# Optimization experiments

Hardware: AMD Instinct MI355X
Metric: run time of the kernel (lower is better)

## Reference

```python
import jax, jax.numpy as jnp
import numpy as np

B, S, D, H, EXP = 4, 2048, 768, 8, 4
HD = D // H  # head dim = 96
EPS = 1e-5


def layer_norm(x, g, b):
    mu = jnp.mean(x, axis=-1, keepdims=True)
    var = jnp.mean(jnp.square(x - mu), axis=-1, keepdims=True)
    return (x - mu) * jax.lax.rsqrt(var + EPS) * g + b


def setup_inputs() -> dict:
    key = jax.random.key(0)
    ks = jax.random.split(key, 16)
    s = 0.02
    f32 = jnp.float32
    x = jax.random.normal(ks[0], (B, S, D), f32)
    Wq = jax.random.normal(ks[1], (D, D), f32) * s
    bq = jnp.zeros((D,), f32)
    Wk = jax.random.normal(ks[2], (D, D), f32) * s
    bk = jnp.zeros((D,), f32)
    Wv = jax.random.normal(ks[3], (D, D), f32) * s
    bv = jnp.zeros((D,), f32)
    Wo = jax.random.normal(ks[4], (D, D), f32) * s
    bo = jnp.zeros((D,), f32)
    g1 = jnp.ones((D,), f32)
    be1 = jnp.zeros((D,), f32)
    W1 = jax.random.normal(ks[5], (D, D * EXP), f32) * s
    bf1 = jnp.zeros((D * EXP,), f32)
    W2 = jax.random.normal(ks[6], (D * EXP, D), f32) * s
    bf2 = jnp.zeros((D,), f32)
    g2 = jnp.ones((D,), f32)
    be2 = jnp.zeros((D,), f32)
    return dict(x=x, Wq=Wq, bq=bq, Wk=Wk, bk=bk, Wv=Wv, bv=bv, Wo=Wo, bo=bo,
                g1=g1, be1=be1, W1=W1, bf1=bf1, W2=W2, bf2=bf2, g2=g2, be2=be2)


def reference(x, Wq, bq, Wk, bk, Wv, bv, Wo, bo, g1, be1, W1, bf1, W2, bf2, g2, be2):
    scale = HD ** (-0.5)
    # multi-head attention (manual QK^T softmax V)
    q = (x @ Wq + bq).reshape(B, S, H, HD).transpose(0, 2, 1, 3)  # b H s c
    k = (x @ Wk + bk).reshape(B, S, H, HD).transpose(0, 2, 1, 3)
    v = (x @ Wv + bv).reshape(B, S, H, HD).transpose(0, 2, 1, 3)
    scores = jnp.einsum('bhqc,bhkc->bhqk', q, k) * scale
    attn = jax.nn.softmax(scores, axis=-1)
    o = jnp.einsum('bhqk,bhkc->bhqc', attn, v)
    o = o.transpose(0, 2, 1, 3).reshape(B, S, D)
    attn_out = o @ Wo + bo
    # residual + LN
    x1 = layer_norm(attn_out + x, g1, be1)
    # feed-forward with GELU
    h = jax.nn.gelu(x1 @ W1 + bf1)
    ffn_out = h @ W2 + bf2
    # residual + LN
    return layer_norm(ffn_out + x1, g2, be2)
```

## Files before the change

kernel.cpp:

```cpp
#include <hip/hip_runtime.h>
#include <hip/hip_bf16.h>
#include <math.h>
#include <stdint.h>

#define B_    4
#define S_    2048
#define D_    768
#define H_    8
#define HD_   96
#define EXPD_ 3072
#define MSZ   8192

#define QSCALE 0.14724439f
#define M0_    12.0f

typedef __bf16 bf16;
typedef __bf16 bf16x4 __attribute__((ext_vector_type(4)));
typedef __bf16 bf16x8 __attribute__((ext_vector_type(8)));
typedef float  f32x4  __attribute__((ext_vector_type(4)));
typedef float  f32x16 __attribute__((ext_vector_type(16)));

typedef __attribute__((address_space(1))) const uint32_t gu32;
typedef __attribute__((address_space(3))) uint32_t lu32;

__device__ __forceinline__ void async_copy16(const void* g, void* l) {
    __builtin_amdgcn_global_load_lds((gu32*)g, (lu32*)l, 16, 0, 0);
}

__device__ __forceinline__ float gelu_f(float x) {
    float x3 = x * x * x;
    return 0.5f * x * (1.0f + tanhf(0.7978845608028654f * (x + 0.044715f * x3)));
}

__device__ __forceinline__ bool sniff_f32(const void* p) {
    const bf16* pb = (const bf16*)p;
    float v = (float)pb[2 * (threadIdx.x & 63)];
    bool big = !(fabsf(v) < 1000.0f);
    return __any(big) != 0;
}

__device__ __forceinline__ float dynld(const void* p, size_t i, bool f32in) {
    return f32in ? ((const float*)p)[i] : (float)((const bf16*)p)[i];
}

__global__ __launch_bounds__(256) void cast_kernel(
    const void* __restrict__ src, bf16* __restrict__ dst)
{
    const bool f32in = sniff_f32(src);
    size_t i = ((size_t)blockIdx.x * 256 + threadIdx.x) * 8;
    if (f32in) {
        f32x4 a = *(const f32x4*)((const float*)src + i);
        f32x4 b = *(const f32x4*)((const float*)src + i + 4);
        bf16x8 r;
#pragma unroll
        for (int e = 0; e < 4; ++e) { r[e] = (bf16)a[e]; r[e + 4] = (bf16)b[e]; }
        *(bf16x8*)(dst + i) = r;
    } else {
        *(bf16x8*)(dst + i) = *(const bf16x8*)((const bf16*)src + i);
    }
}

#define MODE_QKV  0
#define MODE_RES  1
#define MODE_GELU 2

template<int MODE, bool ADYN, bool RESDYN, int BN>
__global__ __launch_bounds__(256) void gemm2_kernel(
    const void* __restrict__ A, const bf16* __restrict__ Bt,
    const void* __restrict__ b0, const void* __restrict__ b1, const void* __restrict__ b2,
    const void* __restrict__ res, bf16* __restrict__ out,
    int M, int N, int K, int lda, int ldb, int boff, int mstripe,
    const void* __restrict__ sniffp)
{
    constexpr int WN   = BN / 2;
    constexpr int NJ32 = WN / 32;
    constexpr int BSZ  = BN * 32;
    __shared__ __align__(16) bf16 Sh[8192 + 2 * BSZ];
    bf16* Asp[2] = { Sh, Sh + 4096 };
    bf16* Bsp[2] = { Sh + 8192, Sh + 8192 + BSZ };

    const bool f32in = sniff_f32(sniffp);
    const int tid  = threadIdx.x;
    const int w    = tid >> 6;
    const int lane = tid & 63;
    const int l32  = lane & 31;
    const int kh   = lane >> 5;
    const int wr   = w >> 1, wc = w & 1;

    const int lin  = blockIdx.x;
    const int xcd  = lin & 7;
    const int q    = lin >> 3;
    const int nb   = q / mstripe;
    const int mbin = q - nb * mstripe;
    const int m0   = (xcd * mstripe + mbin) * 128;
    const int n0   = nb * BN;

    const int rsub = lane >> 2;
    const int cb8  = (lane & 3) * 8;

    f32x16 acc[2][NJ32];
#pragma unroll
    for (int i = 0; i < 2; ++i)
#pragma unroll
        for (int j = 0; j < NJ32; ++j)
#pragma unroll
            for (int e = 0; e < 16; ++e) acc[i][j][e] = 0.f;

    const bf16*  Abf = (const bf16*)A;
    const float* Af  = (const float*)A;

    for (int k0 = 0; k0 < K; k0 += 64) {
        __syncthreads();
#pragma unroll
        for (int half = 0; half < 2; ++half) {
            if (ADYN && f32in) {
#pragma unroll
                for (int a = 0; a < 2; ++a) {
                    int row = w * 32 + a * 16 + rsub;
                    const float* sp = Af + (size_t)(m0 + row) * lda + k0 + half * 32 + cb8;
                    f32x4 u0 = *(const f32x4*)sp;
                    f32x4 u1 = *(const f32x4*)(sp + 4);
                    bf16x8 v;
#pragma unroll
                    for (int e = 0; e < 4; ++e) { v[e] = (bf16)u0[e]; v[e + 4] = (bf16)u1[e]; }
                    *(bf16x8*)(&Asp[half][(size_t)(w * 32 + a * 16) * 32 + lane * 8]) = v;
                }
            } else {
#pragma unroll
                for (int a = 0; a < 2; ++a) {
                    int row = w * 32 + a * 16 + rsub;
                    async_copy16(Abf + (size_t)(m0 + row) * lda + k0 + half * 32 + cb8,
                                 &Asp[half][(w * 32 + a * 16) * 32]);
                }
            }
#pragma unroll
            for (int a = 0; a < BN / 64; ++a) {
                int row = w * (BN / 4) + a * 16 + rsub;
                async_copy16(Bt + (size_t)(n0 + row) * ldb + k0 + half * 32 + cb8,
                             &Bsp[half][(w * (BN / 4) + a * 16) * 32]);
            }
        }
        __syncthreads();

#pragma unroll
        for (int hs = 0; hs < 2; ++hs) {
            bf16x8 af[2][2], bfv[NJ32][2];
#pragma unroll
            for (int i = 0; i < 2; ++i)
#pragma unroll
                for (int ks = 0; ks < 2; ++ks)
                    af[i][ks] = *(const bf16x8*)(&Asp[hs][(wr * 64 + i * 32 + l32) * 32 + ks * 16 + kh * 8]);
#pragma unroll
            for (int j = 0; j < NJ32; ++j)
#pragma unroll
                for (int ks = 0; ks < 2; ++ks)
                    bfv[j][ks] = *(const bf16x8*)(&Bsp[hs][(wc * WN + j * 32 + l32) * 32 + ks * 16 + kh * 8]);
#pragma unroll
            for (int i = 0; i < 2; ++i)
#pragma unroll
                for (int j = 0; j < NJ32; ++j)
#pragma unroll
                    for (int ks = 0; ks < 2; ++ks)
                        acc[i][j] = __builtin_amdgcn_mfma_f32_32x32x16_bf16(af[i][ks], bfv[j][ks], acc[i][j], 0, 0, 0);
        }
    }

    if constexpr (MODE == MODE_QKV) {
#pragma unroll
        for (int j = 0; j < NJ32; ++j) {
            int nbase = n0 + wc * WN + j * 32;
            int which = nbase / D_;
            int n2b   = nbase - which * D_;
            int h     = n2b / HD_;
            int hd0   = n2b - h * HD_;
            const void* bp = which == 0 ? b0 : (which == 1 ? b1 : b2);
            float bval = dynld(bp, n2b + l32, f32in);
            int hd = hd0 + l32;
#pragma unroll
            for (int i = 0; i < 2; ++i) {
#pragma unroll
                for (int g = 0; g < 16; ++g) {
                    int rr = (g & 3) + 8 * (g >> 2) + 4 * kh;
                    int m  = m0 + wr * 64 + i * 32 + rr;
                    float v = acc[i][j][g] + bval;
                    int b  = m >> 11;
                    int ss = m & (S_ - 1);
                    int bh = b * H_ + h;
                    if (which == 0) v *= QSCALE;
                    size_t dst;
                    if (which < 2)
                        dst = (size_t)which * (MSZ * D_) + ((size_t)bh * S_ + ss) * HD_ + hd;
                    else
                        dst = (size_t)2 * (MSZ * D_) + ((size_t)bh * HD_ + hd) * S_ + ss;
                    out[dst] = (bf16)v;
                }
            }
        }
    } else {
        __syncthreads();
        bf16* Cw = Sh + w * 2048;
        for (int j = 0; j < NJ32; ++j) {
            int nl = n0 + wc * WN + j * 32 + l32;
            float bval = boff >= 0 ? dynld(b0, boff + nl, f32in) : 0.f;
#pragma unroll
            for (int i = 0; i < 2; ++i)
#pragma unroll
                for (int g = 0; g < 16; ++g) {
                    int rr = (g & 3) + 8 * (g >> 2) + 4 * kh;
                    float v = acc[i][j][g] + bval;
                    if constexpr (MODE == MODE_GELU) v = gelu_f(v);
                    Cw[(i * 32 + rr) * 32 + l32] = (bf16)v;
                }
#pragma unroll
            for (int pass = 0; pass < 4; ++pass) {
                int row = pass * 16 + (lane >> 2);
                int cc  = (lane & 3) * 8;
                bf16x8 cv = *(const bf16x8*)&Cw[row * 32 + cc];
                int m = m0 + wr * 64 + row;
                int n = n0 + wc * WN + j * 32 + cc;
                size_t off = (size_t)m * N + n;
                if constexpr (MODE == MODE_RES) {
                    bf16x8 o;
                    if (RESDYN && f32in) {
                        f32x4 r0 = *(const f32x4*)((const float*)res + off);
                        f32x4 r1 = *(const f32x4*)((const float*)res + off + 4);
#pragma unroll
                        for (int e = 0; e < 4; ++e) {
                            o[e]     = (bf16)((float)cv[e] + r0[e]);
                            o[e + 4] = (bf16)((float)cv[e + 4] + r1[e]);
                        }
                    } else {
                        bf16x8 rv = *(const bf16x8*)((const bf16*)res + off);
#pragma unroll
                        for (int e = 0; e < 8; ++e) o[e] = (bf16)((float)cv[e] + (float)rv[e]);
                    }
                    *(bf16x8*)&out[off] = o;
                } else {
                    *(bf16x8*)&out[off] = cv;
                }
            }
        }
    }
}

__global__ __launch_bounds__(256, 2) void flash_kernel(
    const bf16* __restrict__ Q, const bf16* __restrict__ Kk,
    const bf16* __restrict__ Vt_g, bf16* __restrict__ ctx)
{
    __shared__ __align__(16) bf16 Ks[64][104];
    __shared__ __align__(16) bf16 Vs[96][72];
    __shared__ __align__(16) bf16 Ps[4][32][72];

    const int tid  = threadIdx.x;
    const int w    = tid >> 6;
    const int lane = tid & 63;
    const int quad = lane >> 4;
    const int l16  = lane & 15;
    const int bh   = blockIdx.x;
    const size_t base = (size_t)bh * S_ * HD_;
    const int q0   = blockIdx.y * 128 + w * 32;

    bf16x8 qf[2][3];
#pragma unroll
    for (int qs = 0; qs < 2; ++qs)
#pragma unroll
        for (int ch = 0; ch < 3; ++ch)
            qf[qs][ch] = *(const bf16x8*)(Q + base + (size_t)(q0 + qs * 16 + l16) * HD_ + ch * 32 + quad * 8);

    f32x4 oacc[2][6];
#pragma unroll
    for (int qs = 0; qs < 2; ++qs)
#pragma unroll
        for (int c = 0; c < 6; ++c) oacc[qs][c] = (f32x4){0.f, 0.f, 0.f, 0.f};
    float lsum[2] = {0.f, 0.f};

    int krow[3], kc8[3], vrow[3], vc8[3];
#pragma unroll
    for (int i = 0; i < 3; ++i) {
        int id = tid + i * 256;
        krow[i] = id / 12; kc8[i] = (id - krow[i] * 12) * 8;
        vrow[i] = id >> 3; vc8[i] = (id & 7) * 8;
    }

    bf16x8 kreg[3], vreg[3];
#pragma unroll
    for (int i = 0; i < 3; ++i) {
        kreg[i] = *(const bf16x8*)(Kk + base + (size_t)krow[i] * HD_ + kc8[i]);
        vreg[i] = *(const bf16x8*)(Vt_g + base + (size_t)vrow[i] * S_ + vc8[i]);
    }
#pragma unroll
    for (int i = 0; i < 3; ++i) {
        *(bf16x8*)(&Ks[krow[i]][kc8[i]]) = kreg[i];
        *(bf16x8*)(&Vs[vrow[i]][vc8[i]]) = vreg[i];
    }
    __syncthreads();

    for (int kv0 = 0; kv0 < S_; kv0 += 64) {
        const bool more = (kv0 + 64) < S_;
        if (more) {
#pragma unroll
            for (int i = 0; i < 3; ++i) {
                kreg[i] = *(const bf16x8*)(Kk + base + (size_t)(kv0 + 64 + krow[i]) * HD_ + kc8[i]);
                vreg[i] = *(const bf16x8*)(Vt_g + base + (size_t)vrow[i] * S_ + kv0 + 64 + vc8[i]);
            }
        }

        f32x4 sacc[2][4];
#pragma unroll
        for (int qs = 0; qs < 2; ++qs)
#pragma unroll
            for (int t = 0; t < 4; ++t)
                sacc[qs][t] = (f32x4){-M0_, -M0_, -M0_, -M0_};
#pragma unroll
        for (int t = 0; t < 4; ++t)
#pragma unroll
            for (int ch = 0; ch < 3; ++ch) {
                bf16x8 kf = *(const bf16x8*)(&Ks[t * 16 + l16][ch * 32 + quad * 8]);
                sacc[0][t] = __builtin_amdgcn_mfma_f32_16x16x32_bf16(kf, qf[0][ch], sacc[0][t], 0, 0, 0);
                sacc[1][t] = __builtin_amdgcn_mfma_f32_16x16x32_bf16(kf, qf[1][ch], sacc[1][t], 0, 0, 0);
            }

#pragma unroll
        for (int qs = 0; qs < 2; ++qs) {
            bf16* prow = &Ps[w][qs * 16 + l16][quad * 4];
#pragma unroll
            for (int t = 0; t < 4; ++t) {
                float p0 = exp2f(sacc[qs][t][0]);
                float p1 = exp2f(sacc[qs][t][1]);
                float p2 = exp2f(sacc[qs][t][2]);
                float p3 = exp2f(sacc[qs][t][3]);
                lsum[qs] += (p0 + p1) + (p2 + p3);
                bf16x4 pv;
                pv[0] = (bf16)p0; pv[1] = (bf16)p1; pv[2] = (bf16)p2; pv[3] = (bf16)p3;
                *(bf16x4*)(prow + t * 16) = pv;
            }
        }

        bf16x8 pf[2][2];
#pragma unroll
        for (int qs = 0; qs < 2; ++qs) {
            pf[qs][0] = *(const bf16x8*)(&Ps[w][qs * 16 + l16][quad * 8]);
            pf[qs][1] = *(const bf16x8*)(&Ps[w][qs * 16 + l16][32 + quad * 8]);
        }
#pragma unroll
        for (int c = 0; c < 6; ++c) {
            bf16x8 vf0 = *(const bf16x8*)(&Vs[c * 16 + l16][quad * 8]);
            bf16x8 vf1 = *(const bf16x8*)(&Vs[c * 16 + l16][32 + quad * 8]);
            oacc[0][c] = __builtin_amdgcn_mfma_f32_16x16x32_bf16(pf[0][0], vf0, oacc[0][c], 0, 0, 0);
            oacc[0][c] = __builtin_amdgcn_mfma_f32_16x16x32_bf16(pf[0][1], vf1, oacc[0][c], 0, 0, 0);
            oacc[1][c] = __builtin_amdgcn_mfma_f32_16x16x32_bf16(pf[1][0], vf0, oacc[1][c], 0, 0, 0);
            oacc[1][c] = __builtin_amdgcn_mfma_f32_16x16x32_bf16(pf[1][1], vf1, oacc[1][c], 0, 0, 0);
        }

        if (more) {
            __syncthreads();
#pragma unroll
            for (int i = 0; i < 3; ++i) {
                *(bf16x8*)(&Ks[krow[i]][kc8[i]]) = kreg[i];
                *(bf16x8*)(&Vs[vrow[i]][vc8[i]]) = vreg[i];
            }
            __syncthreads();
        }
    }

#pragma unroll
    for (int qs = 0; qs < 2; ++qs) {
        lsum[qs] += __shfl_xor(lsum[qs], 16);
        lsum[qs] += __shfl_xor(lsum[qs], 32);
    }
    const int b = bh >> 3, h = bh & 7;
#pragma unroll
    for (int qs = 0; qs < 2; ++qs)
#pragma unroll
        for (int r = 0; r < 4; ++r) {
            float inv = 1.0f / __shfl(lsum[qs], quad * 4 + r);
            int srow = q0 + qs * 16 + quad * 4 + r;
            size_t rowbase = ((size_t)b * S_ + srow) * D_ + h * HD_;
#pragma unroll
            for (int c = 0; c < 6; ++c)
                ctx[rowbase + c * 16 + l16] = (bf16)(oacc[qs][c][r] * inv);
        }
}

template<bool OUTDYN>
__global__ __launch_bounds__(256) void ln_kernel(
    const bf16* __restrict__ in, const void* __restrict__ g, const void* __restrict__ be,
    void* __restrict__ out, const void* __restrict__ sniffp)
{
    const bool f32in = sniff_f32(sniffp);
    const int w = threadIdx.x >> 6, lane = threadIdx.x & 63;
    const int row = blockIdx.x * 4 + w;
    const size_t rbase = (size_t)row * D_ + lane * 12;

    float v[12];
#pragma unroll
    for (int j = 0; j < 3; ++j) {
        bf16x4 t = *(const bf16x4*)(in + rbase + j * 4);
#pragma unroll
        for (int e = 0; e < 4; ++e) v[j * 4 + e] = (float)t[e];
    }
    float sum = 0.f;
#pragma unroll
    for (int j = 0; j < 12; ++j) sum += v[j];
#pragma unroll
    for (int off = 1; off < 64; off <<= 1) sum += __shfl_xor(sum, off);
    float mu = sum * (1.0f / D_);
    float sq = 0.f;
#pragma unroll
    for (int j = 0; j < 12; ++j) { v[j] -= mu; sq += v[j] * v[j]; }
#pragma unroll
    for (int off = 1; off < 64; off <<= 1) sq += __shfl_xor(sq, off);
    float rstd = rsqrtf(sq * (1.0f / D_) + 1e-5f);

    if (OUTDYN && f32in) {
        float* op = (float*)out + rbase;
#pragma unroll
        for (int j = 0; j < 3; ++j) {
            f32x4 t;
#pragma unroll
            for (int e = 0; e < 4; ++e) {
                int c = lane * 12 + j * 4 + e;
                t[e] = v[j * 4 + e] * rstd * dynld(g, c, true) + dynld(be, c, true);
            }
            *(f32x4*)(op + j * 4) = t;
        }
    } else {
        bf16* op = (bf16*)out + rbase;
#pragma unroll
        for (int j = 0; j < 3; ++j) {
            bf16x4 t;
#pragma unroll
            for (int e = 0; e < 4; ++e) {
                int c = lane * 12 + j * 4 + e;
                t[e] = (bf16)(v[j * 4 + e] * rstd * dynld(g, c, f32in) + dynld(be, c, f32in));
            }
            *(bf16x4*)(op + j * 4) = t;
        }
    }
}

__device__ __forceinline__ void transpose_tile(
    const void* __restrict__ src, bf16* __restrict__ dst, int R, int C,
    int r0, int c0, bool f32in)
{
    __shared__ bf16 t[64][65];
    const int tx = threadIdx.x & 63, ty = threadIdx.x >> 6;
#pragma unroll
    for (int i = 0; i < 16; ++i) {
        int rr = ty + i * 4;
        t[rr][tx] = (bf16)dynld(src, (size_t)(r0 + rr) * C + c0 + tx, f32in);
    }
    __syncthreads();
#pragma unroll
    for (int i = 0; i < 16; ++i) {
        int cc = ty + i * 4;
        dst[(size_t)(c0 + cc) * R + r0 + tx] = t[tx][cc];
    }
}

__global__ __launch_bounds__(256) void transpose_qkv_kernel(
    const void* __restrict__ s0, const void* __restrict__ s1, const void* __restrict__ s2,
    bf16* __restrict__ dst)
{
    const void* src = blockIdx.z == 0 ? s0 : (blockIdx.z == 1 ? s1 : s2);
    const bool f32in = sniff_f32(src);
    transpose_tile(src, dst + (size_t)blockIdx.z * D_ * D_, D_, D_,
                   blockIdx.y * 64, blockIdx.x * 64, f32in);
}

__global__ __launch_bounds__(256) void transpose_mlp_kernel(
    const void* __restrict__ s0, const void* __restrict__ s1, const void* __restrict__ s2,
    bf16* __restrict__ dst)
{
    int id = blockIdx.x;
    const void* src;
    int R, C, r, c;
    size_t off;
    if (id < 144)      { src = s0; R = D_;    C = D_;    off = 0;
                         r = id / 12;          c = id % 12; }
    else if (id < 720) { src = s1; R = D_;    C = EXPD_; off = (size_t)D_ * D_;
                         int i = id - 144;     r = i / 48; c = i % 48; }
    else               { src = s2; R = EXPD_; C = D_;    off = (size_t)D_ * D_ + (size_t)D_ * EXPD_;
                         int i = id - 720;     r = i / 12; c = i % 12; }
    const bool f32in = sniff_f32(src);
    transpose_tile(src, dst + off, R, C, r * 64, c * 64, f32in);
}

extern "C" void kernel_launch(void* const* d_in, const int* in_sizes, int n_in,
                              void* d_out, int out_size, void* d_ws, size_t ws_size,
                              hipStream_t stream)
{
    (void)in_sizes; (void)n_in; (void)out_size;
    const void* x   = d_in[0];
    const void* Wq  = d_in[1];
    const void* bq  = d_in[2];
    const void* Wk  = d_in[3];
    const void* bk  = d_in[4];
    const void* Wv  = d_in[5];
    const void* bv  = d_in[6];
    const void* Wo  = d_in[7];
    const void* bo  = d_in[8];
    const void* g1  = d_in[9];
    const void* be1 = d_in[10];
    const void* W1  = d_in[11];
    const void* bf1 = d_in[12];
    const void* W2  = d_in[13];
    const void* bf2 = d_in[14];
    const void* g2  = d_in[15];
    const void* be2 = d_in[16];

    const size_t REG = (size_t)MSZ * D_ * 2;
    char* p = (char*)d_ws;
    bf16* R0 = (bf16*)p;
    bf16* R1 = (bf16*)(p + REG);
    bf16* R2 = (bf16*)(p + 2 * REG);
    bf16* R3 = (bf16*)(p + 3 * REG);
    bf16* R4 = (bf16*)(p + 4 * REG);

    int tier = 0;
    if      (ws_size >= 9 * REG) tier = 3;
    else if (ws_size >= 5 * REG) tier = 1;
    bf16* xb = tier == 3 ? (bf16*)(p + 8 * REG) : R4;

    bf16* qkvT = (bf16*)d_out;
    bf16* ctx  = (bf16*)d_out;
    dim3 blk(256);
    const int MB8 = MSZ / 128 / 8;

    if (tier >= 1) cast_kernel<<<dim3(MSZ * D_ / (256 * 8)), blk, 0, stream>>>(x, xb);

    transpose_qkv_kernel<<<dim3(12, 12, 3), blk, 0, stream>>>(Wq, Wk, Wv, qkvT);

    if (tier >= 1)
        gemm2_kernel<MODE_QKV, false, false, 128><<<dim3(64 * 18), blk, 0, stream>>>(
            xb, qkvT, bq, bk, bv, nullptr, R0, MSZ, 2304, D_, D_, D_, 0, MB8, Wq);
    else
        gemm2_kernel<MODE_QKV, true, false, 128><<<dim3(64 * 18), blk, 0, stream>>>(
            x, qkvT, bq, bk, bv, nullptr, R0, MSZ, 2304, D_, D_, D_, 0, MB8, Wq);

    flash_kernel<<<dim3(B_ * H_, S_ / 128), dim3(256), 0, stream>>>(R0, R1, R2, ctx);

    bf16* WoT = R1;
    bf16* W1T = WoT + (size_t)D_ * D_;
    bf16* W2T = W1T + (size_t)D_ * EXPD_;
    transpose_mlp_kernel<<<dim3(1296), blk, 0, stream>>>(Wo, W1, W2, WoT);

    if (tier >= 1)
        gemm2_kernel<MODE_RES, false, false, 64><<<dim3(64 * 12), blk, 0, stream>>>(
            ctx, WoT, bo, nullptr, nullptr, xb, R3, MSZ, D_, D_, D_, D_, 0, MB8, Wq);
    else
        gemm2_kernel<MODE_RES, false, true, 64><<<dim3(64 * 12), blk, 0, stream>>>(
            ctx, WoT, bo, nullptr, nullptr, x, R3, MSZ, D_, D_, D_, D_, 0, MB8, Wq);

    bf16* x1b = R0;
    ln_kernel<false><<<dim3(MSZ / 4), blk, 0, stream>>>(R3, g1, be1, x1b, Wq);

    bf16* y2b;
    if (tier == 3) {
        bf16* hb = R4;
        y2b = R3;
        gemm2_kernel<MODE_GELU, false, false, 128><<<dim3(64 * 24), blk, 0, stream>>>(
            x1b, W1T, bf1, nullptr, nullptr, nullptr, hb, MSZ, EXPD_, D_, D_, D_, 0, MB8, Wq);
        gemm2_kernel<MODE_RES, false, false, 64><<<dim3(64 * 12), blk, 0, stream>>>(
            hb, W2T, bf2, nullptr, nullptr, x1b, y2b, MSZ, D_, EXPD_, EXPD_, EXPD_, 0, MB8, Wq);
    } else if (tier == 1) {
        bf16* hb = R2;
        y2b = R4;
        gemm2_kernel<MODE_GELU, false, false, 128><<<dim3(64 * 12), blk, 0, stream>>>(
            x1b, W1T, bf1, nullptr, nullptr, nullptr, hb, MSZ, 1536, D_, D_, D_, 0, MB8, Wq);
        gemm2_kernel<MODE_RES, false, false, 64><<<dim3(64 * 12), blk, 0, stream>>>(
            hb, W2T, bf2, nullptr, nullptr, x1b, y2b, MSZ, D_, 1536, 1536, EXPD_, 0, MB8, Wq);
        gemm2_kernel<MODE_GELU, false, false, 128><<<dim3(64 * 12), blk, 0, stream>>>(
            x1b, W1T + (size_t)1536 * D_, bf1, nullptr, nullptr, nullptr, hb, MSZ, 1536, D_, D_, D_, 1536, MB8, Wq);
        gemm2_kernel<MODE_RES, false, false, 64><<<dim3(64 * 12), blk, 0, stream>>>(
            hb, W2T + 1536, nullptr, nullptr, nullptr, y2b, y2b, MSZ, D_, 1536, 1536, EXPD_, -1, MB8, Wq);
    } else {
        bf16* hb = R3;
        y2b = R2;
        const int CH = 2048;
        for (int c0 = 0; c0 < MSZ; c0 += CH) {
            const bf16* x1c = x1b + (size_t)c0 * D_;
            gemm2_kernel<MODE_GELU, false, false, 128><<<dim3(16 * 24), blk, 0, stream>>>(
                x1c, W1T, bf1, nullptr, nullptr, nullptr, hb, CH, EXPD_, D_, D_, D_, 0, 2, Wq);
            gemm2_kernel<MODE_RES, false, false, 64><<<dim3(16 * 12), blk, 0, stream>>>(
                hb, W2T, bf2, nullptr, nullptr, x1c, y2b + (size_t)c0 * D_, CH, D_, EXPD_, EXPD_, EXPD_, 0, 2, Wq);
        }
    }

    ln_kernel<true><<<dim3(MSZ / 4), blk, 0, stream>>>(y2b, g2, be2, d_out, Wq);
}
```

Baseline: 455.1 us.

## Double-buffer GEMM k-loop staging and vectorize QKV epilogue stores through LDS

Restructures the GEMM main loop so the next 64-wide k tile is issued into a second shared-memory buffer while MFMAs run on the current one, removing one barrier per iteration and overlapping loads with compute. The QKV epilogue now stages each 32x32 accumulator tile in LDS and writes Q/K rows and the transposed V rows as 16-byte vectors instead of scattered scalar bf16 stores. This doubles the shared-memory footprint, which may reduce occupancy. The per-lane V gather from LDS may also cause bank conflicts.

```diff
diff --git a/kernel.cpp b/kernel.cpp
--- a/kernel.cpp
+++ b/kernel.cpp
@@ -74,10 +74,10 @@
 {
     constexpr int WN   = BN / 2;
     constexpr int NJ32 = WN / 32;
-    constexpr int BSZ  = BN * 32;
-    __shared__ __align__(16) bf16 Sh[8192 + 2 * BSZ];
-    bf16* Asp[2] = { Sh, Sh + 4096 };
-    bf16* Bsp[2] = { Sh + 8192, Sh + 8192 + BSZ };
+    constexpr int ABUF = 8192;
+    constexpr int BBUF = BN * 64;
+    constexpr int BUF  = ABUF + BBUF;
+    __shared__ __align__(16) bf16 Sh[2 * BUF];
 
     const bool f32in = sniff_f32(sniffp);
     const int tid  = threadIdx.x;
@@ -109,39 +109,49 @@
     const bf16*  Abf = (const bf16*)A;
     const float* Af  = (const float*)A;
 
-    for (int k0 = 0; k0 < K; k0 += 64) {
-        __syncthreads();
+    auto stage = [&](int k0, int bsel) {
+        bf16* As = Sh + bsel * BUF;
+        bf16* Bs = As + ABUF;
 #pragma unroll
         for (int half = 0; half < 2; ++half) {
             if (ADYN && f32in) {
 #pragma unroll
                 for (int a = 0; a < 2; ++a) {
-                    int row = w * 32 + a * 16 + rsub;
-                    const float* sp = Af + (size_t)(m0 + row) * lda + k0 + half * 32 + cb8;
+                    const float* sp = Af + (size_t)(m0 + w * 32 + a * 16 + rsub) * lda + k0 + half * 32 + cb8;
                     f32x4 u0 = *(const f32x4*)sp;
                     f32x4 u1 = *(const f32x4*)(sp + 4);
                     bf16x8 v;
 #pragma unroll
                     for (int e = 0; e < 4; ++e) { v[e] = (bf16)u0[e]; v[e + 4] = (bf16)u1[e]; }
-                    *(bf16x8*)(&Asp[half][(size_t)(w * 32 + a * 16) * 32 + lane * 8]) = v;
+                    *(bf16x8*)(&As[(size_t)(half * 4096) + (size_t)(w * 32 + a * 16) * 32 + lane * 8]) = v;
                 }
             } else {
 #pragma unroll
                 for (int a = 0; a < 2; ++a) {
                     int row = w * 32 + a * 16 + rsub;
                     async_copy16(Abf + (size_t)(m0 + row) * lda + k0 + half * 32 + cb8,
-                                 &Asp[half][(w * 32 + a * 16) * 32]);
+                                 &As[half * 4096 + (w * 32 + a * 16) * 32]);
                 }
             }
 #pragma unroll
             for (int a = 0; a < BN / 64; ++a) {
                 int row = w * (BN / 4) + a * 16 + rsub;
                 async_copy16(Bt + (size_t)(n0 + row) * ldb + k0 + half * 32 + cb8,
-                             &Bsp[half][(w * (BN / 4) + a * 16) * 32]);
-            }
-        }
-        __syncthreads();
-
+                             &Bs[half * (BN * 32) + (w * (BN / 4) + a * 16) * 32]);
+            }
+        }
+    };
+
+    stage(0, 0);
+    __syncthreads();
+
+    const int nk = K >> 6;
+    for (int t = 0; t < nk; ++t) {
+        const int cur = t & 1;
+        if (t + 1 < nk) stage((t + 1) << 6, cur ^ 1);
+
+        const bf16* As = Sh + cur * BUF;
+        const bf16* Bs = As + ABUF;
 #pragma unroll
         for (int hs = 0; hs < 2; ++hs) {
             bf16x8 af[2][2], bfv[NJ32][2];
@@ -149,12 +159,12 @@
             for (int i = 0; i < 2; ++i)
 #pragma unroll
                 for (int ks = 0; ks < 2; ++ks)
-                    af[i][ks] = *(const bf16x8*)(&Asp[hs][(wr * 64 + i * 32 + l32) * 32 + ks * 16 + kh * 8]);
+                    af[i][ks] = *(const bf16x8*)(&As[hs * 4096 + (wr * 64 + i * 32 + l32) * 32 + ks * 16 + kh * 8]);
 #pragma unroll
             for (int j = 0; j < NJ32; ++j)
 #pragma unroll
                 for (int ks = 0; ks < 2; ++ks)
-                    bfv[j][ks] = *(const bf16x8*)(&Bsp[hs][(wc * WN + j * 32 + l32) * 32 + ks * 16 + kh * 8]);
+                    bfv[j][ks] = *(const bf16x8*)(&Bs[hs * (BN * 32) + (wc * WN + j * 32 + l32) * 32 + ks * 16 + kh * 8]);
 #pragma unroll
             for (int i = 0; i < 2; ++i)
 #pragma unroll
@@ -163,9 +173,12 @@
                     for (int ks = 0; ks < 2; ++ks)
                         acc[i][j] = __builtin_amdgcn_mfma_f32_32x32x16_bf16(af[i][ks], bfv[j][ks], acc[i][j], 0, 0, 0);
         }
+        __syncthreads();
     }
 
     if constexpr (MODE == MODE_QKV) {
+        bf16* Cw = Sh + w * 2048;
+        const int bb = (m0 + wr * 64) >> 11;
 #pragma unroll
         for (int j = 0; j < NJ32; ++j) {
             int nbase = n0 + wc * WN + j * 32;
@@ -175,29 +188,41 @@
             int hd0   = n2b - h * HD_;
             const void* bp = which == 0 ? b0 : (which == 1 ? b1 : b2);
             float bval = dynld(bp, n2b + l32, f32in);
-            int hd = hd0 + l32;
-#pragma unroll
-            for (int i = 0; i < 2; ++i) {
+            const int bh = bb * H_ + h;
+#pragma unroll
+            for (int i = 0; i < 2; ++i)
 #pragma unroll
                 for (int g = 0; g < 16; ++g) {
                     int rr = (g & 3) + 8 * (g >> 2) + 4 * kh;
-                    int m  = m0 + wr * 64 + i * 32 + rr;
                     float v = acc[i][j][g] + bval;
-                    int b  = m >> 11;
-                    int ss = m & (S_ - 1);
-                    int bh = b * H_ + h;
                     if (which == 0) v *= QSCALE;
-                    size_t dst;
-                    if (which < 2)
-                        dst = (size_t)which * (MSZ * D_) + ((size_t)bh * S_ + ss) * HD_ + hd;
-                    else
-                        dst = (size_t)2 * (MSZ * D_) + ((size_t)bh * HD_ + hd) * S_ + ss;
-                    out[dst] = (bf16)v;
+                    Cw[(i * 32 + rr) * 32 + l32] = (bf16)v;
                 }
+            if (which < 2) {
+#pragma unroll
+                for (int pass = 0; pass < 4; ++pass) {
+                    int row = pass * 16 + (lane >> 2);
+                    int c8  = (lane & 3) * 8;
+                    bf16x8 cv = *(const bf16x8*)&Cw[row * 32 + c8];
+                    int ss = (m0 + wr * 64 + row) & (S_ - 1);
+                    size_t dst = (size_t)which * (MSZ * D_) + ((size_t)bh * S_ + ss) * HD_ + hd0 + c8;
+                    *(bf16x8*)&out[dst] = cv;
+                }
+            } else {
+                int hd  = hd0 + l32;
+                int ss0 = (m0 + wr * 64) & (S_ - 1);
+                size_t rowb = (size_t)2 * (MSZ * D_) + ((size_t)bh * HD_ + hd) * S_ + ss0 + kh * 32;
+#pragma unroll
+                for (int oct = 0; oct < 4; ++oct) {
+                    bf16x8 cv;
+#pragma unroll
+                    for (int e = 0; e < 8; ++e)
+                        cv[e] = Cw[(kh * 32 + oct * 8 + e) * 32 + l32];
+                    *(bf16x8*)&out[rowb + oct * 8] = cv;
+                }
             }
         }
     } else {
-        __syncthreads();
         bf16* Cw = Sh + w * 2048;
         for (int j = 0; j < NJ32; ++j) {
             int nl = n0 + wc * WN + j * 32 + l32;
```

Result: no change. 449.7 us (-1.2%).
